# Optimization experiments

Hardware: AMD Instinct MI355X
Metric: run time of the kernel (lower is better)

Reference implementation:

```python
import jax, jax.numpy as jnp
import numpy as np

N_NODES = 50000
N_EDGES = 800000
IN_C, HID_C, OUT_C = 128, 128, 64
BN_EPS = 1e-5


def setup_inputs() -> dict:
    key = jax.random.key(0)
    ks = jax.random.split(key, 12)
    def lin(k, fan_in, fan_out):
        bound = 1.0 / np.sqrt(fan_in)
        kw, kb = jax.random.split(k)
        W = jax.random.uniform(kw, (fan_in, fan_out), jnp.float32, -bound, bound)
        b = jax.random.uniform(kb, (fan_out,), jnp.float32, -bound, bound)
        return W, b
    x = jax.random.normal(ks[0], (N_NODES, IN_C), jnp.float32)
    edge_index = jax.random.randint(ks[1], (2, N_EDGES), 0, N_NODES, jnp.int32)
    w1a, b1a = lin(ks[2], IN_C, HID_C)
    w1b, b1b = lin(ks[3], HID_C, HID_C)
    w2a, b2a = lin(ks[4], HID_C, OUT_C)
    w2b, b2b = lin(ks[5], OUT_C, OUT_C)
    return {
        "x": x, "edge_index": edge_index,
        "w1a": w1a, "b1a": b1a, "g1": jnp.ones((HID_C,)), "be1": jnp.zeros((HID_C,)),
        "w1b": w1b, "b1b": b1b,
        "w2a": w2a, "b2a": b2a, "g2": jnp.ones((OUT_C,)), "be2": jnp.zeros((OUT_C,)),
        "w2b": w2b, "b2b": b2b,
    }


def _batchnorm(h, gamma, beta):
    # training-style BN over node dim, biased variance (torch BatchNorm1d)
    mean = jnp.mean(h, axis=0)
    var = jnp.mean(jnp.square(h - mean), axis=0)
    return (h - mean) * jax.lax.rsqrt(var + BN_EPS) * gamma + beta


def _gin_layer(x, src, dst, n_nodes, w_a, b_a, gamma, beta, w_b, b_b):
    # GINConv with eps=0: MLP(x + sum_{j->i} x_j)
    agg = jax.ops.segment_sum(x[src], dst, num_segments=n_nodes)  # [N, C]
    h = x + agg
    h = h @ w_a + b_a
    h = jax.nn.relu(_batchnorm(h, gamma, beta))
    return h @ w_b + b_b


def reference(x, edge_index, w1a, b1a, g1, be1, w1b, b1b, w2a, b2a, g2, be2, w2b, b2b):
    src, dst = edge_index[0], edge_index[1]
    n = x.shape[0]
    h = _gin_layer(x, src, dst, n, w1a, b1a, g1, be1, w1b, b1b)
    h = jax.nn.relu(h)  # dropout p=0.0 -> identity
    h = _gin_layer(h, src, dst, n, w2a, b2a, g2, be2, w2b, b2b)
    return jax.nn.log_softmax(h, axis=-1)
```

## Files before the change

### kernel.cpp

```cpp
#include <hip/hip_runtime.h>


typedef unsigned short u16;
typedef unsigned int u32;
typedef __attribute__((ext_vector_type(8))) short short8;
typedef __attribute__((ext_vector_type(4))) short short4v;
typedef __attribute__((ext_vector_type(4))) float f32x4;

#define DEV_INLINE __device__ __forceinline__

DEV_INLINE void atomAddF(float* p, float v) { unsafeAtomicAdd(p, v); }

DEV_INLINE u16 f2bf(float f) {
    unsigned u = __float_as_uint(f);
    u += 0x7fffu + ((u >> 16) & 1u);
    return (u16)(u >> 16);
}
DEV_INLINE float bf2f(u16 h) { return __uint_as_float(((unsigned)h) << 16); }

__global__ __launch_bounds__(256) void wprep4_k(
    const float* __restrict__ w1a, const float* __restrict__ w1b,
    const float* __restrict__ w2a, const float* __restrict__ w2b,
    short* __restrict__ o1a, short* __restrict__ o1b,
    short* __restrict__ o2a, short* __restrict__ o2b)
{
    int b = blockIdx.x;
    const float* W; short* wf; int K, NOUT;
    if (b < 8)       { W = w1a; wf = o1a; K = 128; NOUT = 128; }
    else if (b < 16) { W = w1b; wf = o1b; K = 128; NOUT = 128; b -= 8; }
    else if (b < 20) { W = w2a; wf = o2a; K = 128; NOUT = 64;  b -= 16; }
    else             { W = w2b; wf = o2b; K = 64;  NOUT = 64;  b -= 20; }
    const int u = b * 256 + threadIdx.x;
    const int units = (NOUT / 16) * (K / 32) * 64;
    if (u >= units) return;
    const int per_ct = (K / 32) * 64;
    const int ct = u / per_ct;
    const int rem = u % per_ct;
    const int kc = rem >> 6;
    const int l = rem & 63;
    const int col = ct * 16 + (l & 15);
    const int k0 = kc * 32 + (l >> 4) * 8;
    short8 pk;
#pragma unroll
    for (int j = 0; j < 8; j++)
        pk[j] = (short)f2bf(W[(size_t)(k0 + j) * NOUT + col]);
    *(short8*)&wf[(size_t)u * 8] = pk;
}

template <int KD, int NC, bool ABF16, bool BNIN, bool BIAS, bool RELUOUT,
          bool LOGSM, bool OBF16>
__global__ __launch_bounds__(256) void mgemm(
    const void* __restrict__ Ap, const short* __restrict__ Wf,
    const float* __restrict__ sum, const float* __restrict__ sumsq,
    const float* __restrict__ g, const float* __restrict__ be, float invN,
    const float* __restrict__ bias, void* __restrict__ outp, int M)
{
    constexpr int BM = 64;
    constexpr int KC = KD / 32;
    constexpr int CT = NC / 16;
    constexpr int KQ = KD / 4;
    __shared__ short Asl[BM * KD];
    __shared__ short Bsl[NC * KD];
    __shared__ float scb[BNIN ? KD : 1];
    __shared__ float shb[BNIN ? KD : 1];

    const int t = threadIdx.x;
    const int l = t & 63;
    const int w = t >> 6;

    if constexpr (BNIN) {
        if (t < KD) {
            const float m = sum[t] * invN;
            const float v = sumsq[t] * invN - m * m;
            const float r = rsqrtf(v + 1e-5f);
            const float s = g[t] * r;
            scb[t] = s;
            shb[t] = be[t] - m * s;
        }
        __syncthreads();
    }

    {
        const float4* src = (const float4*)Wf;
        float4* dst = (float4*)Bsl;
        constexpr int NU = NC * KD / 8;
#pragma unroll
        for (int u = t; u < NU; u += 256) dst[u] = src[u];
    }
    {
        const int r = t >> 2;
        const int q = t & 3;
        const int grow = blockIdx.x * BM + r;
        const int rt = r >> 4;
        u16 hv[KQ];
        if (grow < M) {
            if constexpr (ABF16) {
                const u16* ap = (const u16*)Ap + (size_t)grow * KD + q * KQ;
#pragma unroll
                for (int i = 0; i < KQ / 8; i++)
                    *(short8*)&hv[i * 8] = ((const short8*)ap)[i];
                if constexpr (BNIN) {
#pragma unroll
                    for (int i = 0; i < KQ; i++) {
                        const int k = q * KQ + i;
                        hv[i] = f2bf(fmaxf(0.f, bf2f(hv[i]) * scb[k] + shb[k]));
                    }
                }
            } else {
                const float* ap = (const float*)Ap + (size_t)grow * KD + q * KQ;
#pragma unroll
                for (int i = 0; i < KQ / 4; i++) {
                    const float4 v = ((const float4*)ap)[i];
                    float f0 = v.x, f1 = v.y, f2 = v.z, f3 = v.w;
                    if constexpr (BNIN) {
                        const int k = q * KQ + i * 4;
                        f0 = fmaxf(0.f, f0 * scb[k + 0] + shb[k + 0]);
                        f1 = fmaxf(0.f, f1 * scb[k + 1] + shb[k + 1]);
                        f2 = fmaxf(0.f, f2 * scb[k + 2] + shb[k + 2]);
                        f3 = fmaxf(0.f, f3 * scb[k + 3] + shb[k + 3]);
                    }
                    hv[i * 4 + 0] = f2bf(f0); hv[i * 4 + 1] = f2bf(f1);
                    hv[i * 4 + 2] = f2bf(f2); hv[i * 4 + 3] = f2bf(f3);
                }
            }
        } else {
#pragma unroll
            for (int i = 0; i < KQ; i++) hv[i] = 0;
        }
#pragma unroll
        for (int gg = 0; gg < KQ / 8; gg++) {
            const int k0 = q * KQ + gg * 8;
            const int kc = k0 >> 5;
            const int lane = (r & 15) + ((k0 >> 3) & 3) * 16;
            *(short8*)&Asl[((rt * KC + kc) * 64 + lane) * 8] =
                *(short8*)&hv[gg * 8];
        }
    }
    __syncthreads();

    f32x4 acc[CT];
#pragma unroll
    for (int c = 0; c < CT; c++) acc[c] = (f32x4){0.f, 0.f, 0.f, 0.f};

#pragma unroll
    for (int kc = 0; kc < KC; kc++) {
        const short8 x0 = *(const short8*)&Asl[((w * KC + kc) * 64 + l) * 8];
#pragma unroll
        for (int ct = 0; ct < CT; ct++) {
            const short8 wb = *(const short8*)&Bsl[((ct * KC + kc) * 64 + l) * 8];
            acc[ct] = __builtin_amdgcn_mfma_f32_16x16x32_bf16(wb, x0, acc[ct], 0, 0, 0);
        }
    }

    const int cbase = (l >> 4) * 4;
    const int grow = blockIdx.x * BM + w * 16 + (l & 15);
    if constexpr (!LOGSM) {
        if (grow < M) {
#pragma unroll
            for (int ct = 0; ct < CT; ct++) {
                f32x4 o = acc[ct];
                if constexpr (BIAS) {
                    const float4 bv = *(const float4*)&bias[ct * 16 + cbase];
                    o[0] += bv.x; o[1] += bv.y; o[2] += bv.z; o[3] += bv.w;
                }
                if constexpr (RELUOUT) {
#pragma unroll
                    for (int j = 0; j < 4; j++) o[j] = fmaxf(o[j], 0.f);
                }
                if constexpr (OBF16) {
                    short4v o16;
#pragma unroll
                    for (int j = 0; j < 4; j++) o16[j] = (short)f2bf(o[j]);
                    *(short4v*)&((u16*)outp)[(size_t)grow * NC + ct * 16 + cbase] = o16;
                } else {
                    *(f32x4*)&((float*)outp)[(size_t)grow * NC + ct * 16 + cbase] = o;
                }
            }
        }
    } else {
        float v[CT * 4];
#pragma unroll
        for (int ct = 0; ct < CT; ct++) {
            const float4 bv = *(const float4*)&bias[ct * 16 + cbase];
            v[ct * 4 + 0] = acc[ct][0] + bv.x;
            v[ct * 4 + 1] = acc[ct][1] + bv.y;
            v[ct * 4 + 2] = acc[ct][2] + bv.z;
            v[ct * 4 + 3] = acc[ct][3] + bv.w;
        }
        float m = v[0];
#pragma unroll
        for (int j = 1; j < CT * 4; j++) m = fmaxf(m, v[j]);
        m = fmaxf(m, __shfl_xor(m, 16));
        m = fmaxf(m, __shfl_xor(m, 32));
        float s = 0.f;
#pragma unroll
        for (int j = 0; j < CT * 4; j++) s += __expf(v[j] - m);
        s += __shfl_xor(s, 16);
        s += __shfl_xor(s, 32);
        const float lg = m + __logf(s);
        if (grow < M) {
#pragma unroll
            for (int ct = 0; ct < CT; ct++) {
                f32x4 o;
#pragma unroll
                for (int j = 0; j < 4; j++) o[j] = v[ct * 4 + j] - lg;
                *(f32x4*)&((float*)outp)[(size_t)grow * NC + ct * 16 + cbase] = o;
            }
        }
    }
}

__global__ __launch_bounds__(256) void mgemm23_k(
    const u16* __restrict__ s1, const short* __restrict__ w1bf,
    const short* __restrict__ w2af,
    const float* __restrict__ sum, const float* __restrict__ sumsq,
    const float* __restrict__ g, const float* __restrict__ be, float invN,
    const float* __restrict__ b1b, u16* __restrict__ p2, int M)
{
    constexpr int BM = 64, KD = 128, NC = 128, NO = 64;
    constexpr int KC = KD / 32;
    constexpr int CT = NC / 16;
    constexpr int CT2 = NO / 16;
    constexpr int KQ = KD / 4;
    __shared__ short Asl[BM * KD];
    __shared__ short Bsl[NC * KD];
    __shared__ float scb[KD];
    __shared__ float shb[KD];

    const int t = threadIdx.x;
    const int l = t & 63;
    const int w = t >> 6;

    if (t < KD) {
        const float m = sum[t] * invN;
        const float v = sumsq[t] * invN - m * m;
        const float r = rsqrtf(v + 1e-5f);
        const float s = g[t] * r;
        scb[t] = s;
        shb[t] = be[t] - m * s;
    }
    __syncthreads();

    {
        const float4* src = (const float4*)w1bf;
        float4* dst = (float4*)Bsl;
#pragma unroll
        for (int u = t; u < NC * KD / 8; u += 256) dst[u] = src[u];
    }
    {
        const int r = t >> 2;
        const int q = t & 3;
        const int grow = blockIdx.x * BM + r;
        const int rt = r >> 4;
        u16 hv[KQ];
        if (grow < M) {
            const u16* ap = s1 + (size_t)grow * KD + q * KQ;
#pragma unroll
            for (int i = 0; i < KQ / 8; i++)
                *(short8*)&hv[i * 8] = ((const short8*)ap)[i];
#pragma unroll
            for (int i = 0; i < KQ; i++) {
                const int k = q * KQ + i;
                hv[i] = f2bf(fmaxf(0.f, bf2f(hv[i]) * scb[k] + shb[k]));
            }
        } else {
#pragma unroll
            for (int i = 0; i < KQ; i++) hv[i] = 0;
        }
#pragma unroll
        for (int gg = 0; gg < KQ / 8; gg++) {
            const int k0 = q * KQ + gg * 8;
            const int kc = k0 >> 5;
            const int lane = (r & 15) + ((k0 >> 3) & 3) * 16;
            *(short8*)&Asl[((rt * KC + kc) * 64 + lane) * 8] =
                *(short8*)&hv[gg * 8];
        }
    }
    __syncthreads();

    f32x4 acc[CT];
#pragma unroll
    for (int c = 0; c < CT; c++) acc[c] = (f32x4){0.f, 0.f, 0.f, 0.f};
#pragma unroll
    for (int kc = 0; kc < KC; kc++) {
        const short8 x0 = *(const short8*)&Asl[((w * KC + kc) * 64 + l) * 8];
#pragma unroll
        for (int ct = 0; ct < CT; ct++) {
            const short8 wb = *(const short8*)&Bsl[((ct * KC + kc) * 64 + l) * 8];
            acc[ct] = __builtin_amdgcn_mfma_f32_16x16x32_bf16(wb, x0, acc[ct], 0, 0, 0);
        }
    }
    __syncthreads();

    {
        const int row = w * 16 + (l & 15);
        const int cb4 = l >> 4;
        const int sw = (row & 7) << 1;
#pragma unroll
        for (int ct = 0; ct < CT; ct++) {
            const float4 bv = *(const float4*)&b1b[ct * 16 + cb4 * 4];
            short4v o16;
            o16[0] = (short)f2bf(fmaxf(acc[ct][0] + bv.x, 0.f));
            o16[1] = (short)f2bf(fmaxf(acc[ct][1] + bv.y, 0.f));
            o16[2] = (short)f2bf(fmaxf(acc[ct][2] + bv.z, 0.f));
            o16[3] = (short)f2bf(fmaxf(acc[ct][3] + bv.w, 0.f));
            const int gsw = (ct * 4 + cb4) ^ sw;
            *(short4v*)&Asl[row * 128 + gsw * 4] = o16;
        }
    }
    {
        const float4* src = (const float4*)w2af;
        float4* dst = (float4*)Bsl;
#pragma unroll
        for (int u = t; u < NO * KD / 8; u += 256) dst[u] = src[u];
    }
    __syncthreads();

    f32x4 acc2[CT2];
#pragma unroll
    for (int c = 0; c < CT2; c++) acc2[c] = (f32x4){0.f, 0.f, 0.f, 0.f};
#pragma unroll
    for (int kc = 0; kc < KC; kc++) {
        const int row = w * 16 + (l & 15);
        const int G = kc * 8 + (l >> 4) * 2;
        const int Gs = G ^ ((row & 7) << 1);
        const short8 x0 = *(const short8*)&Asl[row * 128 + Gs * 4];
#pragma unroll
        for (int ct = 0; ct < CT2; ct++) {
            const short8 wb = *(const short8*)&Bsl[((ct * KC + kc) * 64 + l) * 8];
            acc2[ct] = __builtin_amdgcn_mfma_f32_16x16x32_bf16(wb, x0, acc2[ct], 0, 0, 0);
        }
    }

    {
        const int cbase = (l >> 4) * 4;
        const int grow = blockIdx.x * BM + w * 16 + (l & 15);
        if (grow < M) {
#pragma unroll
            for (int ct = 0; ct < CT2; ct++) {
                short4v o16;
#pragma unroll
                for (int j = 0; j < 4; j++) o16[j] = (short)f2bf(acc2[ct][j]);
                *(short4v*)&p2[(size_t)grow * NO + ct * 16 + cbase] = o16;
            }
        }
    }
}

__global__ __launch_bounds__(256) void hist_k(const int* __restrict__ ei,
                                              int* __restrict__ cnt, int E)
{
    const int gid = blockIdx.x * blockDim.x + threadIdx.x;
    const int stride = gridDim.x * blockDim.x;
    for (int e = gid; e < E; e += stride) atomicAdd(&cnt[ei[E + e]], 1);
}

__global__ __launch_bounds__(256) void bsum_k(const int* __restrict__ cnt,
                                              int* __restrict__ bsum, int N)
{
    __shared__ int ws[4];
    const int i = blockIdx.x * 256 + threadIdx.x;
    int v = (i < N) ? cnt[i] : 0;
    for (int d = 32; d; d >>= 1) v += __shfl_xor(v, d, 64);
    if ((threadIdx.x & 63) == 0) ws[threadIdx.x >> 6] = v;
    __syncthreads();
    if (threadIdx.x == 0) bsum[blockIdx.x] = ws[0] + ws[1] + ws[2] + ws[3];
}

__global__ __launch_bounds__(256) void bscan_k(const int* __restrict__ bsum,
                                               int* __restrict__ bpre, int G1)
{
    __shared__ int part[256];
    const int t = threadIdx.x;
    const int v = (t < G1) ? bsum[t] : 0;
    part[t] = v;
    __syncthreads();
    for (int d = 1; d < 256; d <<= 1) {
        const int u = (t >= d) ? part[t - d] : 0;
        __syncthreads();
        part[t] += u;
        __syncthreads();
    }
    bpre[t] = part[t] - v;
}

__global__ __launch_bounds__(256) void offs_k(const int* __restrict__ cnt,
                                              const int* __restrict__ bpre,
                                              int* __restrict__ off,
                                              int* __restrict__ cursor,
                                              int N, int E)
{
    __shared__ int part[256];
    const int t = threadIdx.x;
    const int i = blockIdx.x * 256 + t;
    const int v = (i < N) ? cnt[i] : 0;
    part[t] = v;
    __syncthreads();
    for (int d = 1; d < 256; d <<= 1) {
        const int u = (t >= d) ? part[t - d] : 0;
        __syncthreads();
        part[t] += u;
        __syncthreads();
    }
    if (i < N) {
        const int o = bpre[blockIdx.x] + part[t] - v;
        off[i] = o;
        cursor[i] = o;
    }
    if (blockIdx.x == 0 && t == 0) off[N] = E;
}

__global__ __launch_bounds__(256) void fill_k(const int* __restrict__ ei,
                                              int* __restrict__ cursor,
                                              int* __restrict__ srcs, int E)
{
    const int gid = blockIdx.x * blockDim.x + threadIdx.x;
    const int stride = gridDim.x * blockDim.x;
    for (int e = gid; e < E; e += stride) {
        const int s = ei[e];
        const int d = ei[E + e];
        const int pos = atomicAdd(&cursor[d], 1);
        srcs[pos] = s;
    }
}

template <int C>
__global__ __launch_bounds__(256) void segsum_bf(
    const u16* __restrict__ p, const int* __restrict__ off,
    const int* __restrict__ srcs, u16* __restrict__ out,
    float* __restrict__ sum, float* __restrict__ sumsq, int N)
{
    constexpr int BLKN = 8;
    constexpr int VPL = C / 64;
    __shared__ float red[4][64][2 * VPL];

    const int wv = threadIdx.x >> 6;
    const int l  = threadIdx.x & 63;
    const int base = blockIdx.x * 4 * BLKN;

    float ss[VPL], qq[VPL];
#pragma unroll
    for (int v = 0; v < VPL; v++) { ss[v] = 0.f; qq[v] = 0.f; }

    for (int i = 0; i < BLKN; i++) {
        const int n = base + i * 4 + wv;
        if (n < N) {
            const int lo = __builtin_amdgcn_readfirstlane(off[n]);
            const int hi = __builtin_amdgcn_readfirstlane(off[n + 1]);
            float acc[VPL];
            if constexpr (VPL == 2) {
                const u32 u = *(const u32*)&p[(size_t)n * C + 2 * l];
                acc[0] = bf2f((u16)u);
                acc[1] = bf2f((u16)(u >> 16));
            } else {
                acc[0] = bf2f(p[(size_t)n * C + l]);
            }
            const int cnt = hi - lo;
            if (cnt > 0) {
                const int last = hi - 1;
                int idx[8];
#pragma unroll
                for (int j = 0; j < 8; j++) idx[j] = srcs[min(lo + j, last)];
                for (int e = lo; e < hi; e += 8) {
                    int nx[8];
#pragma unroll
                    for (int j = 0; j < 8; j++)
                        nx[j] = srcs[min(e + 8 + j, last)];
#pragma unroll
                    for (int j = 0; j < 8; j++) {
                        const bool live = (e + j) < hi;
                        if constexpr (VPL == 2) {
                            const u32 u = *(const u32*)&p[(size_t)idx[j] * C + 2 * l];
                            const float v0 = bf2f((u16)u);
                            const float v1 = bf2f((u16)(u >> 16));
                            acc[0] += live ? v0 : 0.f;
                            acc[1] += live ? v1 : 0.f;
                        } else {
                            const float v = bf2f(p[(size_t)idx[j] * C + l]);
                            acc[0] += live ? v : 0.f;
                        }
                    }
#pragma unroll
                    for (int j = 0; j < 8; j++) idx[j] = nx[j];
                }
            }
            if constexpr (VPL == 2) {
                const u16 r0 = f2bf(acc[0]);
                const u16 r1 = f2bf(acc[1]);
                *(u32*)&out[(size_t)n * C + 2 * l] = (u32)r0 | ((u32)r1 << 16);
                const float f0 = bf2f(r0), f1 = bf2f(r1);
                ss[0] += f0; qq[0] += f0 * f0;
                ss[1] += f1; qq[1] += f1 * f1;
            } else {
                const u16 r = f2bf(acc[0]);
                out[(size_t)n * C + l] = r;
                const float f = bf2f(r);
                ss[0] += f; qq[0] += f * f;
            }
        }
    }

#pragma unroll
    for (int v = 0; v < VPL; v++) {
        red[wv][l][2 * v] = ss[v];
        red[wv][l][2 * v + 1] = qq[v];
    }
    __syncthreads();
    if (wv == 0) {
#pragma unroll
        for (int v = 0; v < VPL; v++) {
            float a = 0.f, b = 0.f;
#pragma unroll
            for (int w2 = 0; w2 < 4; w2++) {
                a += red[w2][l][2 * v];
                b += red[w2][l][2 * v + 1];
            }
            const int ch = (VPL == 2) ? (2 * l + v) : l;
            atomAddF(&sum[ch], a);
            atomAddF(&sumsq[ch], b);
        }
    }
}

extern "C" void kernel_launch(void* const* d_in, const int* in_sizes, int n_in,
                              void* d_out, int out_size, void* d_ws, size_t ws_size,
                              hipStream_t stream)
{
    const float* x   = (const float*)d_in[0];
    const int*   ei  = (const int*)d_in[1];
    const float* w1a = (const float*)d_in[2];
    const float* g1  = (const float*)d_in[4];
    const float* be1 = (const float*)d_in[5];
    const float* w1b = (const float*)d_in[6];
    const float* b1b = (const float*)d_in[7];
    const float* w2a = (const float*)d_in[8];
    const float* g2  = (const float*)d_in[10];
    const float* be2 = (const float*)d_in[11];
    const float* w2b = (const float*)d_in[12];
    const float* b2b = (const float*)d_in[13];
    float* out = (float*)d_out;

    const int N = in_sizes[0] / 128;
    const int E = in_sizes[1] / 2;

    u16* buf1 = (u16*)d_ws;
    u16* buf2 = buf1 + (size_t)N * 128;
    float* stats = (float*)(buf2 + (size_t)N * 128);
    float* sum1 = stats,       *sq1 = stats + 128;
    float* sum2 = stats + 256, *sq2 = stats + 320;
    int* cnt    = (int*)(stats + 1024);
    int* off    = cnt + N;
    int* cursor = off + N + 1;
    int* srcs   = cursor + N;
    int* bsum   = srcs + E;
    int* bpre   = bsum + 256;
    short* w1af = (short*)(bpre + 256);
    short* w1bf = w1af + 128 * 128;
    short* w2af = w1bf + 128 * 128;
    short* w2bf = w2af + 128 * 64;
    u16* p1 = buf1;
    u16* s1 = buf2;
    u16* p2 = buf1;
    u16* s2 = buf2;

    hipMemsetAsync(stats, 0, 1024 * sizeof(float) + (size_t)N * sizeof(int), stream);

    const int G1 = (N + 255) / 256;
    const int gb = (N + 63) / 64;
    const int gs = (N + 31) / 32;
    const float invN = 1.f / N;

    hist_k<<<1024, 256, 0, stream>>>(ei, cnt, E);
    bsum_k<<<G1, 256, 0, stream>>>(cnt, bsum, N);
    bscan_k<<<1, 256, 0, stream>>>(bsum, bpre, G1);
    offs_k<<<G1, 256, 0, stream>>>(cnt, bpre, off, cursor, N, E);
    fill_k<<<1024, 256, 0, stream>>>(ei, cursor, srcs, E);

    wprep4_k<<<22, 256, 0, stream>>>(w1a, w1b, w2a, w2b, w1af, w1bf, w2af, w2bf);

    mgemm<128, 128, false, false, false, false, false, true>
        <<<gb, 256, 0, stream>>>(x, w1af, nullptr, nullptr, nullptr, nullptr,
                                 0.f, nullptr, p1, N);
    segsum_bf<128><<<gs, 256, 0, stream>>>(p1, off, srcs, s1, sum1, sq1, N);

    mgemm23_k<<<gb, 256, 0, stream>>>(s1, w1bf, w2af, sum1, sq1, g1, be1,
                                      invN, b1b, p2, N);

    segsum_bf<64><<<gs, 256, 0, stream>>>(p2, off, srcs, s2, sum2, sq2, N);
    mgemm<64, 64, true, true, true, false, true, false>
        <<<gb, 256, 0, stream>>>(s2, w2bf, sum2, sq2, g2, be2, invN, b2b, out, N);
}
```

Baseline: 300.9 us.

## Hold weight fragments in registers per wave and fuse scan into single-pass decoupled lookback

The 128-wide GEMMs now give each wave a fixed pair of output column tiles across all four row tiles. Each wave keeps its weight fragments in registers loaded straight from global memory, so the full weight matrix is no longer staged in shared memory. This cuts LDS use, which could raise occupancy, and removes the weight copy per block. The three-kernel offset scan becomes one kernel where each block spins on flagged predecessor block sums. That saves two launches but depends on every earlier block being resident or already finished to avoid deadlock.

```diff
diff --git a/kernel.cpp b/kernel.cpp
--- a/kernel.cpp
+++ b/kernel.cpp
@@ -47,81 +47,36 @@
     *(short8*)&wf[(size_t)u * 8] = pk;
 }
 
-template <int KD, int NC, bool ABF16, bool BNIN, bool BIAS, bool RELUOUT,
-          bool LOGSM, bool OBF16>
-__global__ __launch_bounds__(256) void mgemm(
-    const void* __restrict__ Ap, const short* __restrict__ Wf,
-    const float* __restrict__ sum, const float* __restrict__ sumsq,
-    const float* __restrict__ g, const float* __restrict__ be, float invN,
-    const float* __restrict__ bias, void* __restrict__ outp, int M)
-{
-    constexpr int BM = 64;
-    constexpr int KC = KD / 32;
-    constexpr int CT = NC / 16;
-    constexpr int KQ = KD / 4;
-    __shared__ short Asl[BM * KD];
-    __shared__ short Bsl[NC * KD];
-    __shared__ float scb[BNIN ? KD : 1];
-    __shared__ float shb[BNIN ? KD : 1];
-
+__global__ __launch_bounds__(256) void mgemm1_k(
+    const float* __restrict__ x, const short* __restrict__ wf,
+    u16* __restrict__ p1, int M)
+{
+    constexpr int KD = 128, NC = 128, KC = 4, KQ = 32;
+    __shared__ short Asl[64 * KD];
     const int t = threadIdx.x;
     const int l = t & 63;
     const int w = t >> 6;
 
-    if constexpr (BNIN) {
-        if (t < KD) {
-            const float m = sum[t] * invN;
-            const float v = sumsq[t] * invN - m * m;
-            const float r = rsqrtf(v + 1e-5f);
-            const float s = g[t] * r;
-            scb[t] = s;
-            shb[t] = be[t] - m * s;
-        }
-        __syncthreads();
-    }
-
-    {
-        const float4* src = (const float4*)Wf;
-        float4* dst = (float4*)Bsl;
-        constexpr int NU = NC * KD / 8;
-#pragma unroll
-        for (int u = t; u < NU; u += 256) dst[u] = src[u];
-    }
+    short8 B[2][KC];
+#pragma unroll
+    for (int c = 0; c < 2; c++)
+#pragma unroll
+        for (int kc = 0; kc < KC; kc++)
+            B[c][kc] = *(const short8*)&wf[(((w * 2 + c) * KC + kc) * 64 + l) * 8];
+
     {
         const int r = t >> 2;
         const int q = t & 3;
-        const int grow = blockIdx.x * BM + r;
+        const int grow = blockIdx.x * 64 + r;
         const int rt = r >> 4;
         u16 hv[KQ];
         if (grow < M) {
-            if constexpr (ABF16) {
-                const u16* ap = (const u16*)Ap + (size_t)grow * KD + q * KQ;
-#pragma unroll
-                for (int i = 0; i < KQ / 8; i++)
-                    *(short8*)&hv[i * 8] = ((const short8*)ap)[i];
-                if constexpr (BNIN) {
-#pragma unroll
-                    for (int i = 0; i < KQ; i++) {
-                        const int k = q * KQ + i;
-                        hv[i] = f2bf(fmaxf(0.f, bf2f(hv[i]) * scb[k] + shb[k]));
-                    }
-                }
-            } else {
-                const float* ap = (const float*)Ap + (size_t)grow * KD + q * KQ;
-#pragma unroll
-                for (int i = 0; i < KQ / 4; i++) {
-                    const float4 v = ((const float4*)ap)[i];
-                    float f0 = v.x, f1 = v.y, f2 = v.z, f3 = v.w;
-                    if constexpr (BNIN) {
-                        const int k = q * KQ + i * 4;
-                        f0 = fmaxf(0.f, f0 * scb[k + 0] + shb[k + 0]);
-                        f1 = fmaxf(0.f, f1 * scb[k + 1] + shb[k + 1]);
-                        f2 = fmaxf(0.f, f2 * scb[k + 2] + shb[k + 2]);
-                        f3 = fmaxf(0.f, f3 * scb[k + 3] + shb[k + 3]);
-                    }
-                    hv[i * 4 + 0] = f2bf(f0); hv[i * 4 + 1] = f2bf(f1);
-                    hv[i * 4 + 2] = f2bf(f2); hv[i * 4 + 3] = f2bf(f3);
-                }
+            const float* ap = x + (size_t)grow * KD + q * KQ;
+#pragma unroll
+            for (int i = 0; i < KQ / 4; i++) {
+                const float4 v = ((const float4*)ap)[i];
+                hv[i * 4 + 0] = f2bf(v.x); hv[i * 4 + 1] = f2bf(v.y);
+                hv[i * 4 + 2] = f2bf(v.z); hv[i * 4 + 3] = f2bf(v.w);
             }
         } else {
 #pragma unroll
@@ -132,79 +87,37 @@
             const int k0 = q * KQ + gg * 8;
             const int kc = k0 >> 5;
             const int lane = (r & 15) + ((k0 >> 3) & 3) * 16;
-            *(short8*)&Asl[((rt * KC + kc) * 64 + lane) * 8] =
-                *(short8*)&hv[gg * 8];
-        }
-    }
-    __syncthreads();
-
-    f32x4 acc[CT];
-#pragma unroll
-    for (int c = 0; c < CT; c++) acc[c] = (f32x4){0.f, 0.f, 0.f, 0.f};
-
-#pragma unroll
-    for (int kc = 0; kc < KC; kc++) {
-        const short8 x0 = *(const short8*)&Asl[((w * KC + kc) * 64 + l) * 8];
-#pragma unroll
-        for (int ct = 0; ct < CT; ct++) {
-            const short8 wb = *(const short8*)&Bsl[((ct * KC + kc) * 64 + l) * 8];
-            acc[ct] = __builtin_amdgcn_mfma_f32_16x16x32_bf16(wb, x0, acc[ct], 0, 0, 0);
-        }
-    }
+            *(short8*)&Asl[((rt * KC + kc) * 64 + lane) * 8] = *(short8*)&hv[gg * 8];
+        }
+    }
+    __syncthreads();
+
+    f32x4 acc[4][2];
+#pragma unroll
+    for (int rt = 0; rt < 4; rt++)
+#pragma unroll
+        for (int c = 0; c < 2; c++) acc[rt][c] = (f32x4){0.f, 0.f, 0.f, 0.f};
+
+#pragma unroll
+    for (int kc = 0; kc < KC; kc++)
+#pragma unroll
+        for (int rt = 0; rt < 4; rt++) {
+            const short8 x0 = *(const short8*)&Asl[((rt * KC + kc) * 64 + l) * 8];
+            acc[rt][0] = __builtin_amdgcn_mfma_f32_16x16x32_bf16(B[0][kc], x0, acc[rt][0], 0, 0, 0);
+            acc[rt][1] = __builtin_amdgcn_mfma_f32_16x16x32_bf16(B[1][kc], x0, acc[rt][1], 0, 0, 0);
+        }
 
     const int cbase = (l >> 4) * 4;
-    const int grow = blockIdx.x * BM + w * 16 + (l & 15);
-    if constexpr (!LOGSM) {
+#pragma unroll
+    for (int rt = 0; rt < 4; rt++) {
+        const int grow = blockIdx.x * 64 + rt * 16 + (l & 15);
         if (grow < M) {
 #pragma unroll
-            for (int ct = 0; ct < CT; ct++) {
-                f32x4 o = acc[ct];
-                if constexpr (BIAS) {
-                    const float4 bv = *(const float4*)&bias[ct * 16 + cbase];
-                    o[0] += bv.x; o[1] += bv.y; o[2] += bv.z; o[3] += bv.w;
-                }
-                if constexpr (RELUOUT) {
-#pragma unroll
-                    for (int j = 0; j < 4; j++) o[j] = fmaxf(o[j], 0.f);
-                }
-                if constexpr (OBF16) {
-                    short4v o16;
-#pragma unroll
-                    for (int j = 0; j < 4; j++) o16[j] = (short)f2bf(o[j]);
-                    *(short4v*)&((u16*)outp)[(size_t)grow * NC + ct * 16 + cbase] = o16;
-                } else {
-                    *(f32x4*)&((float*)outp)[(size_t)grow * NC + ct * 16 + cbase] = o;
-                }
-            }
-        }
-    } else {
-        float v[CT * 4];
-#pragma unroll
-        for (int ct = 0; ct < CT; ct++) {
-            const float4 bv = *(const float4*)&bias[ct * 16 + cbase];
-            v[ct * 4 + 0] = acc[ct][0] + bv.x;
-            v[ct * 4 + 1] = acc[ct][1] + bv.y;
-            v[ct * 4 + 2] = acc[ct][2] + bv.z;
-            v[ct * 4 + 3] = acc[ct][3] + bv.w;
-        }
-        float m = v[0];
-#pragma unroll
-        for (int j = 1; j < CT * 4; j++) m = fmaxf(m, v[j]);
-        m = fmaxf(m, __shfl_xor(m, 16));
-        m = fmaxf(m, __shfl_xor(m, 32));
-        float s = 0.f;
-#pragma unroll
-        for (int j = 0; j < CT * 4; j++) s += __expf(v[j] - m);
-        s += __shfl_xor(s, 16);
-        s += __shfl_xor(s, 32);
-        const float lg = m + __logf(s);
-        if (grow < M) {
-#pragma unroll
-            for (int ct = 0; ct < CT; ct++) {
-                f32x4 o;
-#pragma unroll
-                for (int j = 0; j < 4; j++) o[j] = v[ct * 4 + j] - lg;
-                *(f32x4*)&((float*)outp)[(size_t)grow * NC + ct * 16 + cbase] = o;
+            for (int c = 0; c < 2; c++) {
+                short4v o16;
+#pragma unroll
+                for (int j = 0; j < 4; j++) o16[j] = (short)f2bf(acc[rt][c][j]);
+                *(short4v*)&p1[(size_t)grow * NC + (w * 2 + c) * 16 + cbase] = o16;
             }
         }
     }
@@ -217,19 +130,25 @@
     const float* __restrict__ g, const float* __restrict__ be, float invN,
     const float* __restrict__ b1b, u16* __restrict__ p2, int M)
 {
-    constexpr int BM = 64, KD = 128, NC = 128, NO = 64;
-    constexpr int KC = KD / 32;
-    constexpr int CT = NC / 16;
-    constexpr int CT2 = NO / 16;
-    constexpr int KQ = KD / 4;
-    __shared__ short Asl[BM * KD];
-    __shared__ short Bsl[NC * KD];
+    constexpr int KD = 128, NC = 128, NO = 64, KC = 4, KQ = 32;
+    __shared__ short Asl[64 * KD];
     __shared__ float scb[KD];
     __shared__ float shb[KD];
 
     const int t = threadIdx.x;
     const int l = t & 63;
     const int w = t >> 6;
+
+    short8 B1[2][KC];
+    short8 B2[KC];
+#pragma unroll
+    for (int c = 0; c < 2; c++)
+#pragma unroll
+        for (int kc = 0; kc < KC; kc++)
+            B1[c][kc] = *(const short8*)&w1bf[(((w * 2 + c) * KC + kc) * 64 + l) * 8];
+#pragma unroll
+    for (int kc = 0; kc < KC; kc++)
+        B2[kc] = *(const short8*)&w2af[((w * KC + kc) * 64 + l) * 8];
 
     if (t < KD) {
         const float m = sum[t] * invN;
@@ -242,15 +161,9 @@
     __syncthreads();
 
     {
-        const float4* src = (const float4*)w1bf;
-        float4* dst = (float4*)Bsl;
-#pragma unroll
-        for (int u = t; u < NC * KD / 8; u += 256) dst[u] = src[u];
-    }
-    {
         const int r = t >> 2;
         const int q = t & 3;
-        const int grow = blockIdx.x * BM + r;
+        const int grow = blockIdx.x * 64 + r;
         const int rt = r >> 4;
         u16 hv[KQ];
         if (grow < M) {
@@ -272,8 +185,135 @@
             const int k0 = q * KQ + gg * 8;
             const int kc = k0 >> 5;
             const int lane = (r & 15) + ((k0 >> 3) & 3) * 16;
-            *(short8*)&Asl[((rt * KC + kc) * 64 + lane) * 8] =
-                *(short8*)&hv[gg * 8];
+            *(short8*)&Asl[((rt * KC + kc) * 64 + lane) * 8] = *(short8*)&hv[gg * 8];
+        }
+    }
+    __syncthreads();
+
+    f32x4 acc[4][2];
+#pragma unroll
+    for (int rt = 0; rt < 4; rt++)
+#pragma unroll
+        for (int c = 0; c < 2; c++) acc[rt][c] = (f32x4){0.f, 0.f, 0.f, 0.f};
+#pragma unroll
+    for (int kc = 0; kc < KC; kc++)
+#pragma unroll
+        for (int rt = 0; rt < 4; rt++) {
+            const short8 x0 = *(const short8*)&Asl[((rt * KC + kc) * 64 + l) * 8];
+            acc[rt][0] = __builtin_amdgcn_mfma_f32_16x16x32_bf16(B1[0][kc], x0, acc[rt][0], 0, 0, 0);
+            acc[rt][1] = __builtin_amdgcn_mfma_f32_16x16x32_bf16(B1[1][kc], x0, acc[rt][1], 0, 0, 0);
+        }
+    __syncthreads();
+
+    {
+        const int cb4 = l >> 4;
+#pragma unroll
+        for (int rt = 0; rt < 4; rt++) {
+            const int row = rt * 16 + (l & 15);
+            const int sw = (row & 7) << 1;
+#pragma unroll
+            for (int c = 0; c < 2; c++) {
+                const int ct = w * 2 + c;
+                const float4 bv = *(const float4*)&b1b[ct * 16 + cb4 * 4];
+                short4v o16;
+                o16[0] = (short)f2bf(fmaxf(acc[rt][c][0] + bv.x, 0.f));
+                o16[1] = (short)f2bf(fmaxf(acc[rt][c][1] + bv.y, 0.f));
+                o16[2] = (short)f2bf(fmaxf(acc[rt][c][2] + bv.z, 0.f));
+                o16[3] = (short)f2bf(fmaxf(acc[rt][c][3] + bv.w, 0.f));
+                const int gsw = (ct * 4 + cb4) ^ sw;
+                *(short4v*)&Asl[row * 128 + gsw * 4] = o16;
+            }
+        }
+    }
+    __syncthreads();
+
+    f32x4 acc2[4];
+#pragma unroll
+    for (int rt = 0; rt < 4; rt++) acc2[rt] = (f32x4){0.f, 0.f, 0.f, 0.f};
+#pragma unroll
+    for (int kc = 0; kc < KC; kc++)
+#pragma unroll
+        for (int rt = 0; rt < 4; rt++) {
+            const int row = rt * 16 + (l & 15);
+            const int G = kc * 8 + (l >> 4) * 2;
+            const int Gs = G ^ ((row & 7) << 1);
+            const short8 x0 = *(const short8*)&Asl[row * 128 + Gs * 4];
+            acc2[rt] = __builtin_amdgcn_mfma_f32_16x16x32_bf16(B2[kc], x0, acc2[rt], 0, 0, 0);
+        }
+
+    {
+        const int cbase = (l >> 4) * 4;
+#pragma unroll
+        for (int rt = 0; rt < 4; rt++) {
+            const int grow = blockIdx.x * 64 + rt * 16 + (l & 15);
+            if (grow < M) {
+                short4v o16;
+#pragma unroll
+                for (int j = 0; j < 4; j++) o16[j] = (short)f2bf(acc2[rt][j]);
+                *(short4v*)&p2[(size_t)grow * NO + w * 16 + cbase] = o16;
+            }
+        }
+    }
+}
+
+__global__ __launch_bounds__(256) void mgemm4_k(
+    const u16* __restrict__ s2, const short* __restrict__ Wf,
+    const float* __restrict__ sum, const float* __restrict__ sumsq,
+    const float* __restrict__ g, const float* __restrict__ be, float invN,
+    const float* __restrict__ bias, float* __restrict__ outp, int M)
+{
+    constexpr int KD = 64, NC = 64, KC = 2, CT = 4, KQ = 16;
+    __shared__ short Asl[64 * KD];
+    __shared__ short Bsl[NC * KD];
+    __shared__ float scb[KD];
+    __shared__ float shb[KD];
+
+    const int t = threadIdx.x;
+    const int l = t & 63;
+    const int w = t >> 6;
+
+    if (t < KD) {
+        const float m = sum[t] * invN;
+        const float v = sumsq[t] * invN - m * m;
+        const float r = rsqrtf(v + 1e-5f);
+        const float s = g[t] * r;
+        scb[t] = s;
+        shb[t] = be[t] - m * s;
+    }
+    __syncthreads();
+
+    {
+        const float4* src = (const float4*)Wf;
+        float4* dst = (float4*)Bsl;
+#pragma unroll
+        for (int u = t; u < NC * KD / 8; u += 256) dst[u] = src[u];
+    }
+    {
+        const int r = t >> 2;
+        const int q = t & 3;
+        const int grow = blockIdx.x * 64 + r;
+        const int rt = r >> 4;
+        u16 hv[KQ];
+        if (grow < M) {
+            const u16* ap = s2 + (size_t)grow * KD + q * KQ;
+#pragma unroll
+            for (int i = 0; i < KQ / 8; i++)
+                *(short8*)&hv[i * 8] = ((const short8*)ap)[i];
+#pragma unroll
+            for (int i = 0; i < KQ; i++) {
+                const int k = q * KQ + i;
+                hv[i] = f2bf(fmaxf(0.f, bf2f(hv[i]) * scb[k] + shb[k]));
+            }
+        } else {
+#pragma unroll
+            for (int i = 0; i < KQ; i++) hv[i] = 0;
+        }
+#pragma unroll
+        for (int gg = 0; gg < KQ / 8; gg++) {
+            const int k0 = q * KQ + gg * 8;
+            const int kc = k0 >> 5;
+            const int lane = (r & 15) + ((k0 >> 3) & 3) * 16;
+            *(short8*)&Asl[((rt * KC + kc) * 64 + lane) * 8] = *(short8*)&hv[gg * 8];
         }
     }
     __syncthreads();
@@ -290,89 +330,62 @@
             acc[ct] = __builtin_amdgcn_mfma_f32_16x16x32_bf16(wb, x0, acc[ct], 0, 0, 0);
         }
     }
-    __syncthreads();
-
-    {
-        const int row = w * 16 + (l & 15);
-        const int cb4 = l >> 4;
-        const int sw = (row & 7) << 1;
+
+    const int cbase = (l >> 4) * 4;
+    const int grow = blockIdx.x * 64 + w * 16 + (l & 15);
+    float v[CT * 4];
+#pragma unroll
+    for (int ct = 0; ct < CT; ct++) {
+        const float4 bv = *(const float4*)&bias[ct * 16 + cbase];
+        v[ct * 4 + 0] = acc[ct][0] + bv.x;
+        v[ct * 4 + 1] = acc[ct][1] + bv.y;
+        v[ct * 4 + 2] = acc[ct][2] + bv.z;
+        v[ct * 4 + 3] = acc[ct][3] + bv.w;
+    }
+    float m = v[0];
+#pragma unroll
+    for (int j = 1; j < CT * 4; j++) m = fmaxf(m, v[j]);
+    m = fmaxf(m, __shfl_xor(m, 16));
+    m = fmaxf(m, __shfl_xor(m, 32));
+    float s = 0.f;
+#pragma unroll
+    for (int j = 0; j < CT * 4; j++) s += __expf(v[j] - m);
+    s += __shfl_xor(s, 16);
+    s += __shfl_xor(s, 32);
+    const float lg = m + __logf(s);
+    if (grow < M) {
 #pragma unroll
         for (int ct = 0; ct < CT; ct++) {
-            const float4 bv = *(const float4*)&b1b[ct * 16 + cb4 * 4];
-            short4v o16;
-            o16[0] = (short)f2bf(fmaxf(acc[ct][0] + bv.x, 0.f));
-            o16[1] = (short)f2bf(fmaxf(acc[ct][1] + bv.y, 0.f));
-            o16[2] = (short)f2bf(fmaxf(acc[ct][2] + bv.z, 0.f));
-            o16[3] = (short)f2bf(fmaxf(acc[ct][3] + bv.w, 0.f));
-            const int gsw = (ct * 4 + cb4) ^ sw;
-            *(short4v*)&Asl[row * 128 + gsw * 4] = o16;
-        }
-    }
-    {
-        const float4* src = (const float4*)w2af;
-        float4* dst = (float4*)Bsl;
-#pragma unroll
-        for (int u = t; u < NO * KD / 8; u += 256) dst[u] = src[u];
-    }
-    __syncthreads();
-
-    f32x4 acc2[CT2];
-#pragma unroll
-    for (int c = 0; c < CT2; c++) acc2[c] = (f32x4){0.f, 0.f, 0.f, 0.f};
-#pragma unroll
-    for (int kc = 0; kc < KC; kc++) {
-        const int row = w * 16 + (l & 15);
-        const int G = kc * 8 + (l >> 4) * 2;
-        const int Gs = G ^ ((row & 7) << 1);
-        const short8 x0 = *(const short8*)&Asl[row * 128 + Gs * 4];
-#pragma unroll
-        for (int ct = 0; ct < CT2; ct++) {
-            const short8 wb = *(const short8*)&Bsl[((ct * KC + kc) * 64 + l) * 8];
-            acc2[ct] = __builtin_amdgcn_mfma_f32_16x16x32_bf16(wb, x0, acc2[ct], 0, 0, 0);
-        }
-    }
-
-    {
-        const int cbase = (l >> 4) * 4;
-        const int grow = blockIdx.x * BM + w * 16 + (l & 15);
-        if (grow < M) {
-#pragma unroll
-            for (int ct = 0; ct < CT2; ct++) {
-                short4v o16;
-#pragma unroll
-                for (int j = 0; j < 4; j++) o16[j] = (short)f2bf(acc2[ct][j]);
-                *(short4v*)&p2[(size_t)grow * NO + ct * 16 + cbase] = o16;
-            }
+            f32x4 o;
+#pragma unroll
+            for (int j = 0; j < 4; j++) o[j] = v[ct * 4 + j] - lg;
+            *(f32x4*)&outp[(size_t)grow * NC + ct * 16 + cbase] = o;
         }
     }
 }
 
 __global__ __launch_bounds__(256) void hist_k(const int* __restrict__ ei,
-                                              int* __restrict__ cnt, int E)
+                                              int* __restrict__ cnt,
+                                              int* __restrict__ agg, int E)
 {
     const int gid = blockIdx.x * blockDim.x + threadIdx.x;
+    if (gid < 256) agg[gid] = 0;
     const int stride = gridDim.x * blockDim.x;
     for (int e = gid; e < E; e += stride) atomicAdd(&cnt[ei[E + e]], 1);
 }
 
-__global__ __launch_bounds__(256) void bsum_k(const int* __restrict__ cnt,
-                                              int* __restrict__ bsum, int N)
-{
-    __shared__ int ws[4];
-    const int i = blockIdx.x * 256 + threadIdx.x;
-    int v = (i < N) ? cnt[i] : 0;
-    for (int d = 32; d; d >>= 1) v += __shfl_xor(v, d, 64);
-    if ((threadIdx.x & 63) == 0) ws[threadIdx.x >> 6] = v;
-    __syncthreads();
-    if (threadIdx.x == 0) bsum[blockIdx.x] = ws[0] + ws[1] + ws[2] + ws[3];
-}
-
-__global__ __launch_bounds__(256) void bscan_k(const int* __restrict__ bsum,
-                                               int* __restrict__ bpre, int G1)
+__global__ __launch_bounds__(256) void scan1_k(const int* __restrict__ cnt,
+                                               int* __restrict__ agg,
+                                               int* __restrict__ off,
+                                               int* __restrict__ cursor,
+                                               int N, int E)
 {
     __shared__ int part[256];
+    __shared__ int redu[256];
     const int t = threadIdx.x;
-    const int v = (t < G1) ? bsum[t] : 0;
+    const int b = blockIdx.x;
+    const int i = b * 256 + t;
+    const int v = (i < N) ? cnt[i] : 0;
     part[t] = v;
     __syncthreads();
     for (int d = 1; d < 256; d <<= 1) {
@@ -381,33 +394,31 @@
         part[t] += u;
         __syncthreads();
     }
-    bpre[t] = part[t] - v;
-}
-
-__global__ __launch_bounds__(256) void offs_k(const int* __restrict__ cnt,
-                                              const int* __restrict__ bpre,
-                                              int* __restrict__ off,
-                                              int* __restrict__ cursor,
-                                              int N, int E)
-{
-    __shared__ int part[256];
-    const int t = threadIdx.x;
-    const int i = blockIdx.x * 256 + t;
-    const int v = (i < N) ? cnt[i] : 0;
-    part[t] = v;
-    __syncthreads();
-    for (int d = 1; d < 256; d <<= 1) {
-        const int u = (t >= d) ? part[t - d] : 0;
+    if (t == 0)
+        __hip_atomic_store(&agg[b], part[255] | (1 << 30), __ATOMIC_RELEASE,
+                           __HIP_MEMORY_SCOPE_AGENT);
+    int loc = 0;
+    for (int pb = t; pb < b; pb += 256) {
+        int a;
+        do {
+            a = __hip_atomic_load(&agg[pb], __ATOMIC_ACQUIRE,
+                                  __HIP_MEMORY_SCOPE_AGENT);
+        } while (!(a & (1 << 30)));
+        loc += a & ((1 << 30) - 1);
+    }
+    redu[t] = loc;
+    __syncthreads();
+    for (int s = 128; s; s >>= 1) {
+        if (t < s) redu[t] += redu[t + s];
         __syncthreads();
-        part[t] += u;
-        __syncthreads();
-    }
+    }
+    const int base = redu[0];
     if (i < N) {
-        const int o = bpre[blockIdx.x] + part[t] - v;
+        const int o = base + part[t] - v;
         off[i] = o;
         cursor[i] = o;
     }
-    if (blockIdx.x == 0 && t == 0) off[N] = E;
+    if (b == 0 && t == 0) off[N] = E;
 }
 
 __global__ __launch_bounds__(256) void fill_k(const int* __restrict__ ei,
@@ -552,8 +563,8 @@
     int* off    = cnt + N;
     int* cursor = off + N + 1;
     int* srcs   = cursor + N;
-    int* bsum   = srcs + E;
-    int* bpre   = bsum + 256;
+    int* agg    = srcs + E;
+    int* bpre   = agg + 256;
     short* w1af = (short*)(bpre + 256);
     short* w1bf = w1af + 128 * 128;
     short* w2af = w1bf + 128 * 128;
@@ -570,23 +581,19 @@
     const int gs = (N + 31) / 32;
     const float invN = 1.f / N;
 
-    hist_k<<<1024, 256, 0, stream>>>(ei, cnt, E);
-    bsum_k<<<G1, 256, 0, stream>>>(cnt, bsum, N);
-    bscan_k<<<1, 256, 0, stream>>>(bsum, bpre, G1);
-    offs_k<<<G1, 256, 0, stream>>>(cnt, bpre, off, cursor, N, E);
+    hist_k<<<1024, 256, 0, stream>>>(ei, cnt, agg, E);
+    scan1_k<<<G1, 256, 0, stream>>>(cnt, agg, off, cursor, N, E);
     fill_k<<<1024, 256, 0, stream>>>(ei, cursor, srcs, E);
 
     wprep4_k<<<22, 256, 0, stream>>>(w1a, w1b, w2a, w2b, w1af, w1bf, w2af, w2bf);
 
-    mgemm<128, 128, false, false, false, false, false, true>
-        <<<gb, 256, 0, stream>>>(x, w1af, nullptr, nullptr, nullptr, nullptr,
-                                 0.f, nullptr, p1, N);
+    mgemm1_k<<<gb, 256, 0, stream>>>(x, w1af, p1, N);
     segsum_bf<128><<<gs, 256, 0, stream>>>(p1, off, srcs, s1, sum1, sq1, N);
 
     mgemm23_k<<<gb, 256, 0, stream>>>(s1, w1bf, w2af, sum1, sq1, g1, be1,
                                       invN, b1b, p2, N);
 
     segsum_bf<64><<<gs, 256, 0, stream>>>(p2, off, srcs, s2, sum2, sq2, N);
-    mgemm<64, 64, true, true, true, false, true, false>
-        <<<gb, 256, 0, stream>>>(s2, w2bf, sum2, sq2, g2, be2, invN, b2b, out, N);
-}
+    mgemm4_k<<<gb, 256, 0, stream>>>(s2, w2bf, sum2, sq2, g2, be2, invN, b2b,
+                                     out, N);
+}
```

After: 290.6 us. 1.04x faster.
